# Performance work log

Hardware: AMD Instinct MI355X
Metric: run time of the kernel (lower is better)

## Reference

```python
import jax, jax.numpy as jnp
import numpy as np

B, S, H, NH = 2, 2048, 768, 12
D = H // NH            # head dim = 64
R = 256                # relative-position buckets (Embedding(256, D))
MAX_REL = 128


def _rel_indices(s):
    # indices[i, j] = clip(j - i, -MAX_REL, MAX_REL - 1) + MAX_REL  in [0, R)
    pos = np.arange(s)
    rel = pos[None, :] - pos[:, None]
    return jnp.asarray(np.clip(rel, -MAX_REL, MAX_REL - 1) + MAX_REL, dtype=jnp.int32)


def setup_inputs() -> dict:
    key = jax.random.key(0)
    ks = jax.random.split(key, 8)
    sc = 0.02
    return {
        "hidden_states": jax.random.normal(ks[0], (B, S, H), jnp.float32),
        "input_mask": jnp.ones((B, S), jnp.float32),
        "Wq": jax.random.normal(ks[1], (H, H), jnp.float32) * sc,
        "bq": jnp.zeros((H,), jnp.float32),
        "Wk": jax.random.normal(ks[2], (H, H), jnp.float32) * sc,
        "bk": jnp.zeros((H,), jnp.float32),
        "Wv": jax.random.normal(ks[3], (H, H), jnp.float32) * sc,
        "bv": jnp.zeros((H,), jnp.float32),
        "rel_key_emb": jax.random.normal(ks[4], (R, D), jnp.float32) * sc,
        "rel_value_emb": jax.random.normal(ks[5], (R, D), jnp.float32) * sc,
        "indices": _rel_indices(S),
    }


def _heads(x):
    # [B, S, H] -> [B, NH, S, D]
    return x.reshape(B, S, NH, D).transpose(0, 2, 1, 3)


def reference(hidden_states, input_mask, Wq, bq, Wk, bk, Wv, bv,
              rel_key_emb, rel_value_emb, indices):
    q = _heads(hidden_states @ Wq + bq)
    k = _heads(hidden_states @ Wk + bk)
    v = _heads(hidden_states @ Wv + bv)

    scale = 1.0 / jnp.sqrt(jnp.asarray(D, hidden_states.dtype))
    scores = jnp.einsum("bhid,bhjd->bhij", q, k) * scale  # [B,NH,S,S]

    # relative position key bias: gather along bucket axis per (i, j)
    rel_scores = jnp.einsum("bhid,rd->bhir", q, rel_key_emb) * scale  # [B,NH,S,R]
    idx = jnp.broadcast_to(indices[None, None], scores.shape)         # [B,NH,S,S]
    scores = scores + jnp.take_along_axis(rel_scores, idx, axis=3)

    mask_bias = (1.0 - input_mask)[:, None, None, :] * -10000.0
    probs = jax.nn.softmax(scores + mask_bias, axis=-1)               # [B,NH,S,S]

    ctx = jnp.einsum("bhij,bhjd->bhid", probs, v)                     # [B,NH,S,D]

    # scatter-add attention probs into relative buckets, then matmul values
    rows = jnp.arange(S)[:, None]  # broadcast with indices [S,S]
    rel_probs = jnp.zeros_like(rel_scores).at[:, :, rows, indices].add(probs)
    ctx = ctx + jnp.einsum("bhir,rd->bhid", rel_probs, rel_value_emb)

    return ctx.transpose(0, 2, 1, 3).reshape(B, S, H)
```

## Files before the change

### kernel.cpp

```cpp
#include <hip/hip_runtime.h>
#include <hip/hip_bf16.h>
#include <math.h>


#define LDS_ATOMIC_ADD(p, v) __hip_atomic_fetch_add((p), (v), __ATOMIC_RELAXED, __HIP_MEMORY_SCOPE_WORKGROUP)

typedef short short8v __attribute__((ext_vector_type(8)));
typedef short short4v __attribute__((ext_vector_type(4)));
typedef float f32x4 __attribute__((ext_vector_type(4)));

#define MFMA16x16x32(a, b, c) __builtin_amdgcn_mfma_f32_16x16x32_bf16((a), (b), (c), 0, 0, 0)

__device__ inline short f2bf(float f) {
  unsigned u = __float_as_uint(f);
  unsigned r = (u + 0x7FFFu + ((u >> 16) & 1u)) >> 16;
  return (short)r;
}
__device__ inline float bf2f(short b) {
  return __uint_as_float(((unsigned)(unsigned short)b) << 16);
}

__global__ __launch_bounds__(256) void prep_wt_kernel(
    const float* __restrict__ Wq, const float* __restrict__ Wk,
    const float* __restrict__ Wv, short* __restrict__ wt) {
  __shared__ float tile[64][65];
  const int t = threadIdx.x, tx = t & 15, ty = t >> 4;
  const int w = blockIdx.z;
  const float* W = (w == 0) ? Wq : (w == 1) ? Wk : Wv;
  const int k0 = blockIdx.x * 64, n0 = blockIdx.y * 64;
  #pragma unroll
  for (int rr = 0; rr < 4; ++rr) {
    const int kr = rr * 16 + ty;
    const float4 v = *(const float4*)&W[(size_t)(k0 + kr) * 768 + n0 + tx * 4];
    tile[kr][tx*4 + 0] = v.x; tile[kr][tx*4 + 1] = v.y;
    tile[kr][tx*4 + 2] = v.z; tile[kr][tx*4 + 3] = v.w;
  }
  __syncthreads();
  #pragma unroll
  for (int rr = 0; rr < 4; ++rr) {
    const int nr = rr * 16 + ty;
    short4v s;
    #pragma unroll
    for (int c = 0; c < 4; ++c) s[c] = f2bf(tile[tx*4 + c][nr]);
    *(short4v*)&wt[((size_t)w * 768 + n0 + nr) * 768 + k0 + tx * 4] = s;
  }
}

__global__ __launch_bounds__(256) void rvet_kernel(
    const float* __restrict__ rve, const float* __restrict__ rke,
    short* __restrict__ rvet, short* __restrict__ rkeb) {
  const int idx = blockIdx.x * 256 + threadIdx.x;
  const int r = idx >> 6, d = idx & 63;
  rvet[d*256 + r] = f2bf(rve[idx]);
  rkeb[idx]       = f2bf(rke[idx]);
}

__global__ __launch_bounds__(256) void qkv_mfma_kernel(
    const float* __restrict__ hs, const short* __restrict__ wt,
    const float* __restrict__ bq, const float* __restrict__ bk,
    const float* __restrict__ bv,
    short* __restrict__ qbf, short* __restrict__ kbf, short* __restrict__ vbf) {
  __shared__ short lds[3 * 8192];
  short* Ah = lds;
  short* Al = lds + 8192;
  short* Bt = lds + 16384;

  const int t = threadIdx.x, lane = t & 63, wv = t >> 6;
  const int wm = wv & 1, wn = wv >> 1;
  const int lrow = lane & 15, g = lane >> 4;
  const int m0 = blockIdx.x * 128, n0 = blockIdx.y * 128, w = blockIdx.z;
  const short* Bg = wt + (size_t)w * 768 * 768;
  const float* bias = (w == 0) ? bq : (w == 1) ? bk : bv;
  short* outp = (w == 0) ? qbf : (w == 1) ? kbf : vbf;

  int srow[4], sc[4];
  #pragma unroll
  for (int e = 0; e < 4; ++e) {
    const int id = t + 256*e;
    srow[e] = id >> 3; sc[e] = id & 7;
  }

  #pragma unroll
  for (int e = 0; e < 4; ++e) {
    const int row = srow[e], c = sc[e];
    const int dst = row*64 + ((c ^ (row & 7)) * 8);
    const float* s = &hs[(size_t)(m0 + row)*768 + c*8];
    const float4 f0 = *(const float4*)s, f1 = *(const float4*)(s + 4);
    float x[8] = {f0.x, f0.y, f0.z, f0.w, f1.x, f1.y, f1.z, f1.w};
    short8v hiv, lov;
    #pragma unroll
    for (int i = 0; i < 8; ++i) {
      hiv[i] = f2bf(x[i]);
      lov[i] = f2bf(x[i] - bf2f(hiv[i]));
    }
    *(short8v*)&Ah[dst] = hiv;
    *(short8v*)&Al[dst] = lov;
    *(short8v*)&Bt[dst] = *(const short8v*)&Bg[(size_t)(n0 + row)*768 + c*8];
  }
  __syncthreads();

  f32x4 acc[4][4] = {};

  for (int kt = 0; kt < 12; ++kt) {
    float4 pf0[4], pf1[4];
    short8v pb[4];
    const bool have_next = (kt < 11);
    if (have_next) {
      const int k0n = (kt + 1) * 64;
      #pragma unroll
      for (int e = 0; e < 4; ++e) {
        const int row = srow[e], c = sc[e];
        const float* s = &hs[(size_t)(m0 + row)*768 + k0n + c*8];
        pf0[e] = *(const float4*)s;
        pf1[e] = *(const float4*)(s + 4);
        pb[e]  = *(const short8v*)&Bg[(size_t)(n0 + row)*768 + k0n + c*8];
      }
    }

    #pragma unroll
    for (int kc = 0; kc < 2; ++kc) {
      short8v af[4], alf[4], bfv[4];
      #pragma unroll
      for (int fm = 0; fm < 4; ++fm) {
        const int row = wm*64 + fm*16 + lrow;
        const int off = row*64 + (((kc*4 + g) ^ (row & 7)) * 8);
        af[fm]  = *(const short8v*)&Ah[off];
        alf[fm] = *(const short8v*)&Al[off];
      }
      #pragma unroll
      for (int fn = 0; fn < 4; ++fn) {
        const int row = wn*64 + fn*16 + lrow;
        bfv[fn] = *(const short8v*)&Bt[row*64 + (((kc*4 + g) ^ (row & 7)) * 8)];
      }
      #pragma unroll
      for (int fm = 0; fm < 4; ++fm)
        #pragma unroll
        for (int fn = 0; fn < 4; ++fn) {
          acc[fm][fn] = MFMA16x16x32(af[fm],  bfv[fn], acc[fm][fn]);
          acc[fm][fn] = MFMA16x16x32(alf[fm], bfv[fn], acc[fm][fn]);
        }
    }
    __syncthreads();
    if (have_next) {
      #pragma unroll
      for (int e = 0; e < 4; ++e) {
        const int row = srow[e], c = sc[e];
        const int dst = row*64 + ((c ^ (row & 7)) * 8);
        float x[8] = {pf0[e].x, pf0[e].y, pf0[e].z, pf0[e].w,
                      pf1[e].x, pf1[e].y, pf1[e].z, pf1[e].w};
        short8v hiv, lov;
        #pragma unroll
        for (int i = 0; i < 8; ++i) {
          hiv[i] = f2bf(x[i]);
          lov[i] = f2bf(x[i] - bf2f(hiv[i]));
        }
        *(short8v*)&Ah[dst] = hiv;
        *(short8v*)&Al[dst] = lov;
        *(short8v*)&Bt[dst] = pb[e];
      }
    }
    __syncthreads();
  }

  float bias_v[4];
  #pragma unroll
  for (int fn = 0; fn < 4; ++fn) bias_v[fn] = bias[n0 + wn*64 + fn*16 + lrow];

  #pragma unroll
  for (int fm = 0; fm < 4; ++fm) {
    #pragma unroll
    for (int r = 0; r < 4; ++r) {
      const int m = m0 + wm*64 + fm*16 + g*4 + r;
      const int b = m >> 11, s = m & 2047;
      #pragma unroll
      for (int fn = 0; fn < 4; ++fn) {
        const int n = n0 + wn*64 + fn*16 + lrow;
        const int h = n >> 6, d = n & 63;
        const size_t bh = (size_t)b*12 + h;
        outp[(bh*2048 + s)*64 + d] = f2bf(acc[fm][fn][r] + bias_v[fn]);
      }
    }
  }
}

__global__ __launch_bounds__(256) void transpose_v_kernel(
    const short* __restrict__ vbf, short* __restrict__ vtbf) {
  __shared__ short tile[64][66];
  const int t = threadIdx.x;
  const int bh = blockIdx.y;
  const int s0 = blockIdx.x * 64;
  const short* src = vbf + ((size_t)bh*2048 + s0)*64;
  const int row = t >> 3, c = t & 7;
  #pragma unroll
  for (int e = 0; e < 2; ++e) {
    const int r = row + 32*e;
    *(short8v*)&tile[r][c*8] = *(const short8v*)&src[(size_t)r*64 + c*8];
  }
  __syncthreads();
  #pragma unroll
  for (int e = 0; e < 2; ++e) {
    const int d = row + 32*e;
    short8v v;
    #pragma unroll
    for (int k = 0; k < 8; ++k) v[k] = tile[c*8 + k][d];
    *(short8v*)&vtbf[((size_t)bh*64 + d)*2048 + s0 + c*8] = v;
  }
}

__global__ __launch_bounds__(256) void attn_mfma_kernel(
    const short* __restrict__ qbf, const short* __restrict__ kbf,
    const short* __restrict__ vtbf, const short* __restrict__ rkeb,
    const short* __restrict__ rvet, const float* __restrict__ mask,
    float* __restrict__ out) {
  __shared__ __align__(16) char smem[53632];
  short* rp_bf   = (short*)smem;
  short* rs_ldsb = (short*)(smem + 16384);
  short* k_lds   = (short*)(smem + 32768);
  short* vt_lds  = (short*)(smem + 40960);
  short* qp_lds  = (short*)(smem + 49152);
  float* l_s     = (float*)(smem + 53248);
  float* edge_f  = (float*)(smem + 53376);

  const int t    = threadIdx.x;
  const int lane = t & 63, wv = t >> 6;
  const int ih   = wv & 1, jh = wv >> 1;
  const int lrow = lane & 15, g = lane >> 4;
  const int swz  = (lrow & 7) << 3;

  const int bh = blockIdx.y, b = bh / 12, h = bh % 12;
  const int i0 = blockIdx.x * 32;

  const short* qb  = qbf  + ((size_t)bh*2048 + i0)*64;
  const short* kb  = kbf  + (size_t)bh*2048*64;
  const short* vtb = vtbf + (size_t)bh*64*2048;
  const float* mb  = mask + (size_t)b*2048;

  {
    const short8v z8 = {0,0,0,0,0,0,0,0};
    #pragma unroll
    for (int e = 0; e < 4; ++e) *(short8v*)&rp_bf[(e*256 + t)*8] = z8;
    if (t < 32) { l_s[t] = 0.f; edge_f[2*t] = 0.f; edge_f[2*t+1] = 0.f; }
  }
  {
    const int row = t >> 3, c = t & 7;
    *(short8v*)&qp_lds[row*64 + ((c ^ (row & 7))*8)] =
        *(const short8v*)&qb[row*64 + c*8];
  }
  #pragma unroll
  for (int e = 0; e < 2; ++e) {
    const int id = t + 256*e, row = id >> 3, c = id & 7;
    *(short8v*)&k_lds[row*64 + ((c ^ (row & 7))*8)] =
        *(const short8v*)&kb[(size_t)row*64 + c*8];
    *(short8v*)&vt_lds[row*64 + ((c ^ (row & 7))*8)] =
        *(const short8v*)&vtb[(size_t)row*2048 + c*8];
  }
  __syncthreads();

  const short8v aq0 = *(const short8v*)&qp_lds[(ih*16 + lrow)*64 + ((g*8) ^ swz)];
  const short8v aq1 = *(const short8v*)&qp_lds[(ih*16 + lrow)*64 + ((32 + g*8) ^ swz)];

  {
    f32x4 racc[2][4] = {};
    #pragma unroll
    for (int kc = 0; kc < 2; ++kc) {
      short8v am0 = *(const short8v*)&qp_lds[lrow*64 + (((kc*4 + g) ^ (lrow & 7))*8)];
      short8v am1 = *(const short8v*)&qp_lds[(16 + lrow)*64 + (((kc*4 + g) ^ ((16 + lrow) & 7))*8)];
      #pragma unroll
      for (int fn = 0; fn < 4; ++fn) {
        const short8v bb = *(const short8v*)&rkeb[(size_t)(wv*64 + fn*16 + lrow)*64 + kc*32 + g*8];
        racc[0][fn] = MFMA16x16x32(am0, bb, racc[0][fn]);
        racc[1][fn] = MFMA16x16x32(am1, bb, racc[1][fn]);
      }
    }
    #pragma unroll
    for (int mt = 0; mt < 2; ++mt)
      #pragma unroll
      for (int fn = 0; fn < 4; ++fn)
        #pragma unroll
        for (int r = 0; r < 4; ++r) {
          const int il = mt*16 + 4*g + r;
          const int bk = wv*64 + fn*16 + lrow;
          rs_ldsb[il*256 + (((bk >> 3) ^ (il & 7)) << 3) + (bk & 7)] =
              f2bf(racc[mt][fn][r] * 0.125f);
        }
  }
  __syncthreads();

  float rs_lo[4], rs_hi[4];
  #pragma unroll
  for (int r = 0; r < 4; ++r) {
    const int il = ih*16 + 4*g + r;
    rs_lo[r] = bf2f(rs_ldsb[il*256 + ((il & 7) << 3)]);
    rs_hi[r] = bf2f(rs_ldsb[il*256 + (((31 ^ (il & 7)) << 3) + 7)]);
  }
  float ls_p[4]  = {0,0,0,0};
  float rpl_p[4] = {0,0,0,0};
  float rph_p[4] = {0,0,0,0};
  f32x4 ctx0 = {0,0,0,0}, ctx1 = {0,0,0,0};

  const int srow0 = t >> 3, sc = t & 7, srow1 = (t >> 3) + 32;
  short8v stk0, stk1, stv0, stv1;

  for (int jt = 0; jt < 32; ++jt) {
    const int j0 = jt * 64;
    const bool have_next = (jt < 31);

    if (jt > 0) {
      *(short8v*)&vt_lds[srow0*64 + ((sc ^ (srow0 & 7))*8)] = stv0;
      *(short8v*)&vt_lds[srow1*64 + ((sc ^ (srow1 & 7))*8)] = stv1;
    }
    if (have_next) {
      const int j0n = j0 + 64;
      stk0 = *(const short8v*)&kb[(size_t)(j0n + srow0)*64 + sc*8];
      stk1 = *(const short8v*)&kb[(size_t)(j0n + srow1)*64 + sc*8];
      stv0 = *(const short8v*)&vtb[(size_t)srow0*2048 + j0n + sc*8];
      stv1 = *(const short8v*)&vtb[(size_t)srow1*2048 + j0n + sc*8];
    }

    f32x4 c0 = {0,0,0,0}, c1 = {0,0,0,0};
    {
      const int jr0 = jh*32 + lrow, jr1 = jh*32 + 16 + lrow;
      const short8v b00 = *(const short8v*)&k_lds[jr0*64 + ((g*8) ^ swz)];
      const short8v b01 = *(const short8v*)&k_lds[jr0*64 + ((32 + g*8) ^ swz)];
      const short8v b10 = *(const short8v*)&k_lds[jr1*64 + ((g*8) ^ swz)];
      const short8v b11 = *(const short8v*)&k_lds[jr1*64 + ((32 + g*8) ^ swz)];
      c0 = MFMA16x16x32(aq0, b00, c0);
      c0 = MFMA16x16x32(aq1, b01, c0);
      c1 = MFMA16x16x32(aq0, b10, c1);
      c1 = MFMA16x16x32(aq1, b11, c1);
    }

    const float m0v = (1.0f - mb[j0 + jh*32 + lrow])      * -10000.0f;
    const float m1v = (1.0f - mb[j0 + jh*32 + 16 + lrow]) * -10000.0f;

    if (j0 <= i0 - 192) {
      #pragma unroll
      for (int r = 0; r < 4; ++r) {
        const int il  = ih*16 + 4*g + r;
        const int wsw = ((4*g + r) & 7) << 3;
        const float p0 = __expf(c0[r]*0.125f + rs_lo[r] + m0v - 8.0f);
        const float p1 = __expf(c1[r]*0.125f + rs_lo[r] + m1v - 8.0f);
        qp_lds[il*64 + ((jh*32 + lrow) ^ wsw)]      = f2bf(p0);
        qp_lds[il*64 + ((jh*32 + 16 + lrow) ^ wsw)] = f2bf(p1);
        rpl_p[r] += p0 + p1; ls_p[r] += p0 + p1;
      }
    } else if (j0 >= i0 + 159) {
      #pragma unroll
      for (int r = 0; r < 4; ++r) {
        const int il  = ih*16 + 4*g + r;
        const int wsw = ((4*g + r) & 7) << 3;
        const float p0 = __expf(c0[r]*0.125f + rs_hi[r] + m0v - 8.0f);
        const float p1 = __expf(c1[r]*0.125f + rs_hi[r] + m1v - 8.0f);
        qp_lds[il*64 + ((jh*32 + lrow) ^ wsw)]      = f2bf(p0);
        qp_lds[il*64 + ((jh*32 + 16 + lrow) ^ wsw)] = f2bf(p1);
        rph_p[r] += p0 + p1; ls_p[r] += p0 + p1;
      }
    } else {
      #pragma unroll
      for (int r = 0; r < 4; ++r) {
        const int il  = ih*16 + 4*g + r;
        const int gi  = i0 + il;
        const int wsw = ((4*g + r) & 7) << 3;
        {
          const int jl = jh*32 + lrow, gj = j0 + jl;
          int rel = gj - gi; rel = rel < -128 ? -128 : (rel > 127 ? 127 : rel);
          const int bk = rel + 128;
          const float rsv = bf2f(rs_ldsb[il*256 + (((bk >> 3) ^ (il & 7)) << 3) + (bk & 7)]);
          const float p = __expf(c0[r]*0.125f + rsv + m0v - 8.0f);
          qp_lds[il*64 + (jl ^ wsw)] = f2bf(p);
          if (bk == 0)        rpl_p[r] += p;
          else if (bk == 255) rph_p[r] += p;
          else rp_bf[il*256 + (((bk >> 3) ^ (il & 7)) << 3) + (bk & 7)] = f2bf(p);
          ls_p[r] += p;
        }
        {
          const int jl = jh*32 + 16 + lrow, gj = j0 + jl;
          int rel = gj - gi; rel = rel < -128 ? -128 : (rel > 127 ? 127 : rel);
          const int bk = rel + 128;
          const float rsv = bf2f(rs_ldsb[il*256 + (((bk >> 3) ^ (il & 7)) << 3) + (bk & 7)]);
          const float p = __expf(c1[r]*0.125f + rsv + m1v - 8.0f);
          qp_lds[il*64 + (jl ^ wsw)] = f2bf(p);
          if (bk == 0)        rpl_p[r] += p;
          else if (bk == 255) rph_p[r] += p;
          else rp_bf[il*256 + (((bk >> 3) ^ (il & 7)) << 3) + (bk & 7)] = f2bf(p);
          ls_p[r] += p;
        }
      }
    }
    __syncthreads();

    if (have_next) {
      *(short8v*)&k_lds[srow0*64 + ((sc ^ (srow0 & 7))*8)] = stk0;
      *(short8v*)&k_lds[srow1*64 + ((sc ^ (srow1 & 7))*8)] = stk1;
    }

    {
      const int prow = ih*16 + lrow;
      const short8v pa0 = *(const short8v*)&qp_lds[prow*64 + ((g*8) ^ swz)];
      const short8v pa1 = *(const short8v*)&qp_lds[prow*64 + ((32 + g*8) ^ swz)];
      const int d0 = jh*32 + lrow, d1 = jh*32 + 16 + lrow;
      const short8v vb00 = *(const short8v*)&vt_lds[d0*64 + ((g*8) ^ swz)];
      const short8v vb01 = *(const short8v*)&vt_lds[d0*64 + ((32 + g*8) ^ swz)];
      const short8v vb10 = *(const short8v*)&vt_lds[d1*64 + ((g*8) ^ swz)];
      const short8v vb11 = *(const short8v*)&vt_lds[d1*64 + ((32 + g*8) ^ swz)];
      ctx0 = MFMA16x16x32(pa0, vb00, ctx0);
      ctx0 = MFMA16x16x32(pa1, vb01, ctx0);
      ctx1 = MFMA16x16x32(pa0, vb10, ctx1);
      ctx1 = MFMA16x16x32(pa1, vb11, ctx1);
    }
    __syncthreads();
  }

  #pragma unroll
  for (int r = 0; r < 4; ++r) {
    float a = ls_p[r], bl = rpl_p[r], bhv = rph_p[r];
    #pragma unroll
    for (int m = 1; m < 16; m <<= 1) {
      a   += __shfl_xor(a, m);
      bl  += __shfl_xor(bl, m);
      bhv += __shfl_xor(bhv, m);
    }
    if (lrow == 0) {
      const int il = ih*16 + 4*g + r;
      LDS_ATOMIC_ADD(&l_s[il], a);
      LDS_ATOMIC_ADD(&edge_f[2*il + 0], bl);
      LDS_ATOMIC_ADD(&edge_f[2*il + 1], bhv);
    }
  }
  __syncthreads();

  if (t < 32) {
    const int row = t;
    rp_bf[row*256 + (((0  ^ (row & 7))) << 3) + 0] = f2bf(edge_f[2*row + 0]);
    rp_bf[row*256 + (((31 ^ (row & 7))) << 3) + 7] = f2bf(edge_f[2*row + 1]);
  }
  __syncthreads();

  {
    const int arow = ih*16 + lrow;
    const int d0 = jh*32 + lrow, d1 = jh*32 + 16 + lrow;
    #pragma unroll
    for (int ks = 0; ks < 8; ++ks) {
      const short8v a  = *(const short8v*)&rp_bf[arow*256 + (((ks*4 + g) ^ (lrow & 7))*8)];
      const short8v b0 = *(const short8v*)&rvet[d0*256 + ks*32 + g*8];
      const short8v b1 = *(const short8v*)&rvet[d1*256 + ks*32 + g*8];
      ctx0 = MFMA16x16x32(a, b0, ctx0);
      ctx1 = MFMA16x16x32(a, b1, ctx1);
    }
  }

  #pragma unroll
  for (int r = 0; r < 4; ++r) {
    const int il = ih*16 + 4*g + r;
    const float invl = 1.0f / l_s[il];
    const int gi = i0 + il;
    out[(size_t)(b*2048 + gi)*768 + h*64 + jh*32 + lrow]      = ctx0[r] * invl;
    out[(size_t)(b*2048 + gi)*768 + h*64 + jh*32 + 16 + lrow] = ctx1[r] * invl;
  }
}

extern "C" void kernel_launch(void* const* d_in, const int* in_sizes, int n_in,
                              void* d_out, int out_size, void* d_ws, size_t ws_size,
                              hipStream_t stream) {
  const float* hs   = (const float*)d_in[0];
  const float* mask = (const float*)d_in[1];
  const float* Wq   = (const float*)d_in[2];
  const float* bq   = (const float*)d_in[3];
  const float* Wk   = (const float*)d_in[4];
  const float* bk   = (const float*)d_in[5];
  const float* Wv   = (const float*)d_in[6];
  const float* bv   = (const float*)d_in[7];
  const float* rke  = (const float*)d_in[8];
  const float* rve  = (const float*)d_in[9];

  const size_t need_bytes = 28770304;
  if (ws_size < need_bytes) return;

  short* p     = (short*)d_ws;
  short* wtb   = p;
  short* qbf   = p + 1769472;
  short* kbf   = p + 4915200;
  short* vbf   = p + 8060928;
  short* vtbf  = p + 11206656;
  short* rvet  = p + 14352384;
  short* rkeb  = p + 14368768;
  float* out   = (float*)d_out;

  prep_wt_kernel<<<dim3(12, 12, 3), dim3(256), 0, stream>>>(Wq, Wk, Wv, wtb);
  rvet_kernel<<<dim3(64), dim3(256), 0, stream>>>(rve, rke, rvet, rkeb);
  qkv_mfma_kernel<<<dim3(32, 6, 3), dim3(256), 0, stream>>>(
      hs, wtb, bq, bk, bv, qbf, kbf, vbf);
  transpose_v_kernel<<<dim3(32, 24), dim3(256), 0, stream>>>(vbf, vtbf);
  attn_mfma_kernel<<<dim3(64, 24), dim3(256), 0, stream>>>(
      qbf, kbf, vtbf, rkeb, rvet, mask, out);
}
```

Baseline: 245.7 us.

## Drop split-bf16 QKV projection and alias relative-score and relative-prob LDS buffers

Result: no change. 249.3 us (+1.5%).

```diff
diff --git a/kernel.cpp b/kernel.cpp
--- a/kernel.cpp
+++ b/kernel.cpp
@@ -60,10 +60,9 @@
     const float* __restrict__ bq, const float* __restrict__ bk,
     const float* __restrict__ bv,
     short* __restrict__ qbf, short* __restrict__ kbf, short* __restrict__ vbf) {
-  __shared__ short lds[3 * 8192];
+  __shared__ short lds[2 * 8192];
   short* Ah = lds;
-  short* Al = lds + 8192;
-  short* Bt = lds + 16384;
+  short* Bt = lds + 8192;
 
   const int t = threadIdx.x, lane = t & 63, wv = t >> 6;
   const int wm = wv & 1, wn = wv >> 1;
@@ -86,15 +85,10 @@
     const int dst = row*64 + ((c ^ (row & 7)) * 8);
     const float* s = &hs[(size_t)(m0 + row)*768 + c*8];
     const float4 f0 = *(const float4*)s, f1 = *(const float4*)(s + 4);
-    float x[8] = {f0.x, f0.y, f0.z, f0.w, f1.x, f1.y, f1.z, f1.w};
-    short8v hiv, lov;
-    #pragma unroll
-    for (int i = 0; i < 8; ++i) {
-      hiv[i] = f2bf(x[i]);
-      lov[i] = f2bf(x[i] - bf2f(hiv[i]));
-    }
+    short8v hiv;
+    hiv[0] = f2bf(f0.x); hiv[1] = f2bf(f0.y); hiv[2] = f2bf(f0.z); hiv[3] = f2bf(f0.w);
+    hiv[4] = f2bf(f1.x); hiv[5] = f2bf(f1.y); hiv[6] = f2bf(f1.z); hiv[7] = f2bf(f1.w);
     *(short8v*)&Ah[dst] = hiv;
-    *(short8v*)&Al[dst] = lov;
     *(short8v*)&Bt[dst] = *(const short8v*)&Bg[(size_t)(n0 + row)*768 + c*8];
   }
   __syncthreads();
@@ -119,13 +113,11 @@
 
     #pragma unroll
     for (int kc = 0; kc < 2; ++kc) {
-      short8v af[4], alf[4], bfv[4];
+      short8v af[4], bfv[4];
       #pragma unroll
       for (int fm = 0; fm < 4; ++fm) {
         const int row = wm*64 + fm*16 + lrow;
-        const int off = row*64 + (((kc*4 + g) ^ (row & 7)) * 8);
-        af[fm]  = *(const short8v*)&Ah[off];
-        alf[fm] = *(const short8v*)&Al[off];
+        af[fm] = *(const short8v*)&Ah[row*64 + (((kc*4 + g) ^ (row & 7)) * 8)];
       }
       #pragma unroll
       for (int fn = 0; fn < 4; ++fn) {
@@ -135,10 +127,8 @@
       #pragma unroll
       for (int fm = 0; fm < 4; ++fm)
         #pragma unroll
-        for (int fn = 0; fn < 4; ++fn) {
-          acc[fm][fn] = MFMA16x16x32(af[fm],  bfv[fn], acc[fm][fn]);
-          acc[fm][fn] = MFMA16x16x32(alf[fm], bfv[fn], acc[fm][fn]);
-        }
+        for (int fn = 0; fn < 4; ++fn)
+          acc[fm][fn] = MFMA16x16x32(af[fm], bfv[fn], acc[fm][fn]);
     }
     __syncthreads();
     if (have_next) {
@@ -146,16 +136,12 @@
       for (int e = 0; e < 4; ++e) {
         const int row = srow[e], c = sc[e];
         const int dst = row*64 + ((c ^ (row & 7)) * 8);
-        float x[8] = {pf0[e].x, pf0[e].y, pf0[e].z, pf0[e].w,
-                      pf1[e].x, pf1[e].y, pf1[e].z, pf1[e].w};
-        short8v hiv, lov;
-        #pragma unroll
-        for (int i = 0; i < 8; ++i) {
-          hiv[i] = f2bf(x[i]);
-          lov[i] = f2bf(x[i] - bf2f(hiv[i]));
-        }
+        short8v hiv;
+        hiv[0] = f2bf(pf0[e].x); hiv[1] = f2bf(pf0[e].y);
+        hiv[2] = f2bf(pf0[e].z); hiv[3] = f2bf(pf0[e].w);
+        hiv[4] = f2bf(pf1[e].x); hiv[5] = f2bf(pf1[e].y);
+        hiv[6] = f2bf(pf1[e].z); hiv[7] = f2bf(pf1[e].w);
         *(short8v*)&Ah[dst] = hiv;
-        *(short8v*)&Al[dst] = lov;
         *(short8v*)&Bt[dst] = pb[e];
       }
     }
@@ -212,14 +198,13 @@
     const short* __restrict__ vtbf, const short* __restrict__ rkeb,
     const short* __restrict__ rvet, const float* __restrict__ mask,
     float* __restrict__ out) {
-  __shared__ __align__(16) char smem[53632];
-  short* rp_bf   = (short*)smem;
-  short* rs_ldsb = (short*)(smem + 16384);
-  short* k_lds   = (short*)(smem + 32768);
-  short* vt_lds  = (short*)(smem + 40960);
-  short* qp_lds  = (short*)(smem + 49152);
-  float* l_s     = (float*)(smem + 53248);
-  float* edge_f  = (float*)(smem + 53376);
+  __shared__ __align__(16) char smem[37248];
+  short* rr_bf   = (short*)smem;
+  short* k_lds   = (short*)(smem + 16384);
+  short* vt_lds  = (short*)(smem + 24576);
+  short* qp_lds  = (short*)(smem + 32768);
+  float* l_s     = (float*)(smem + 36864);
+  float* edge_f  = (float*)(smem + 36992);
 
   const int t    = threadIdx.x;
   const int lane = t & 63, wv = t >> 6;
@@ -235,12 +220,7 @@
   const short* vtb = vtbf + (size_t)bh*64*2048;
   const float* mb  = mask + (size_t)b*2048;
 
-  {
-    const short8v z8 = {0,0,0,0,0,0,0,0};
-    #pragma unroll
-    for (int e = 0; e < 4; ++e) *(short8v*)&rp_bf[(e*256 + t)*8] = z8;
-    if (t < 32) { l_s[t] = 0.f; edge_f[2*t] = 0.f; edge_f[2*t+1] = 0.f; }
-  }
+  if (t < 32) { l_s[t] = 0.f; edge_f[2*t] = 0.f; edge_f[2*t+1] = 0.f; }
   {
     const int row = t >> 3, c = t & 7;
     *(short8v*)&qp_lds[row*64 + ((c ^ (row & 7))*8)] =
@@ -280,7 +260,7 @@
         for (int r = 0; r < 4; ++r) {
           const int il = mt*16 + 4*g + r;
           const int bk = wv*64 + fn*16 + lrow;
-          rs_ldsb[il*256 + (((bk >> 3) ^ (il & 7)) << 3) + (bk & 7)] =
+          rr_bf[il*256 + (((bk >> 3) ^ (il & 7)) << 3) + (bk & 7)] =
               f2bf(racc[mt][fn][r] * 0.125f);
         }
   }
@@ -290,8 +270,8 @@
   #pragma unroll
   for (int r = 0; r < 4; ++r) {
     const int il = ih*16 + 4*g + r;
-    rs_lo[r] = bf2f(rs_ldsb[il*256 + ((il & 7) << 3)]);
-    rs_hi[r] = bf2f(rs_ldsb[il*256 + (((31 ^ (il & 7)) << 3) + 7)]);
+    rs_lo[r] = bf2f(rr_bf[il*256 + ((il & 7) << 3)]);
+    rs_hi[r] = bf2f(rr_bf[il*256 + (((31 ^ (il & 7)) << 3) + 7)]);
   }
   float ls_p[4]  = {0,0,0,0};
   float rpl_p[4] = {0,0,0,0};
@@ -365,24 +345,24 @@
           const int jl = jh*32 + lrow, gj = j0 + jl;
           int rel = gj - gi; rel = rel < -128 ? -128 : (rel > 127 ? 127 : rel);
           const int bk = rel + 128;
-          const float rsv = bf2f(rs_ldsb[il*256 + (((bk >> 3) ^ (il & 7)) << 3) + (bk & 7)]);
-          const float p = __expf(c0[r]*0.125f + rsv + m0v - 8.0f);
+          const int slot = il*256 + (((bk >> 3) ^ (il & 7)) << 3) + (bk & 7);
+          const float p = __expf(c0[r]*0.125f + bf2f(rr_bf[slot]) + m0v - 8.0f);
           qp_lds[il*64 + (jl ^ wsw)] = f2bf(p);
           if (bk == 0)        rpl_p[r] += p;
           else if (bk == 255) rph_p[r] += p;
-          else rp_bf[il*256 + (((bk >> 3) ^ (il & 7)) << 3) + (bk & 7)] = f2bf(p);
+          else rr_bf[slot] = f2bf(p);
           ls_p[r] += p;
         }
         {
           const int jl = jh*32 + 16 + lrow, gj = j0 + jl;
           int rel = gj - gi; rel = rel < -128 ? -128 : (rel > 127 ? 127 : rel);
           const int bk = rel + 128;
-          const float rsv = bf2f(rs_ldsb[il*256 + (((bk >> 3) ^ (il & 7)) << 3) + (bk & 7)]);
-          const float p = __expf(c1[r]*0.125f + rsv + m1v - 8.0f);
+          const int slot = il*256 + (((bk >> 3) ^ (il & 7)) << 3) + (bk & 7);
+          const float p = __expf(c1[r]*0.125f + bf2f(rr_bf[slot]) + m1v - 8.0f);
           qp_lds[il*64 + (jl ^ wsw)] = f2bf(p);
           if (bk == 0)        rpl_p[r] += p;
           else if (bk == 255) rph_p[r] += p;
-          else rp_bf[il*256 + (((bk >> 3) ^ (il & 7)) << 3) + (bk & 7)] = f2bf(p);
+          else rr_bf[slot] = f2bf(p);
           ls_p[r] += p;
         }
       }
@@ -429,10 +409,23 @@
   }
   __syncthreads();
 
+  if (i0 < 128) {
+    for (int id = t; id < 4096; id += 256) {
+      const int row = id >> 7, bk = (id & 127) + 1;
+      if (bk <= 127 - (i0 + row))
+        rr_bf[row*256 + (((bk >> 3) ^ (row & 7)) << 3) + (bk & 7)] = 0;
+    }
+  } else if (i0 >= 1920) {
+    for (int id = t; id < 4096; id += 256) {
+      const int row = id >> 7, bk = 254 - (id & 127);
+      if (bk >= 2176 - (i0 + row))
+        rr_bf[row*256 + (((bk >> 3) ^ (row & 7)) << 3) + (bk & 7)] = 0;
+    }
+  }
   if (t < 32) {
     const int row = t;
-    rp_bf[row*256 + (((0  ^ (row & 7))) << 3) + 0] = f2bf(edge_f[2*row + 0]);
-    rp_bf[row*256 + (((31 ^ (row & 7))) << 3) + 7] = f2bf(edge_f[2*row + 1]);
+    rr_bf[row*256 + ((row & 7) << 3)]              = f2bf(edge_f[2*row + 0]);
+    rr_bf[row*256 + (((31 ^ (row & 7)) << 3) + 7)] = f2bf(edge_f[2*row + 1]);
   }
   __syncthreads();
 
@@ -441,7 +434,7 @@
     const int d0 = jh*32 + lrow, d1 = jh*32 + 16 + lrow;
     #pragma unroll
     for (int ks = 0; ks < 8; ++ks) {
-      const short8v a  = *(const short8v*)&rp_bf[arow*256 + (((ks*4 + g) ^ (lrow & 7))*8)];
+      const short8v a  = *(const short8v*)&rr_bf[arow*256 + (((ks*4 + g) ^ (lrow & 7))*8)];
       const short8v b0 = *(const short8v*)&rvet[d0*256 + ks*32 + g*8];
       const short8v b1 = *(const short8v*)&rvet[d1*256 + ks*32 + g*8];
       ctx0 = MFMA16x16x32(a, b0, ctx0);
```
